# Optimization experiments

Hardware: AMD Instinct MI355X
Metric: run time of the kernel (lower is better)

## Reference

```python
import jax, jax.numpy as jnp
import numpy as np

B, F_IN, T_IN = 256, 3, 800
C, K, H, N_OUT = 128, 15, 150, 10

def hard_sigmoid(x):
    # Keras-style hard sigmoid used by LSTMHardSigmoid: clamp(0.2*x + 0.5, 0, 1)
    return jnp.clip(0.2 * x + 0.5, 0.0, 1.0)

def setup_inputs() -> dict:
    key = jax.random.key(0)
    ks = jax.random.split(key, 16)
    mk = lambda k, s, sc=0.05: (jax.random.normal(k, s, dtype=jnp.float32) * sc)
    return {
        "x": jax.random.normal(ks[0], (B, F_IN, T_IN), dtype=jnp.float32),
        "conv_w": mk(ks[1], (C, F_IN, K), 0.1),
        "conv_b": jnp.zeros((C,), jnp.float32),
        # PyTorch LSTM layout: [4H, in] with gate order i,f,g,o
        "w_ih_f": mk(ks[2], (4 * H, C)),
        "w_hh_f": mk(ks[3], (4 * H, H)),
        "b_ih_f": mk(ks[4], (4 * H,)),
        "b_hh_f": mk(ks[5], (4 * H,)),
        "w_ih_b": mk(ks[6], (4 * H, C)),
        "w_hh_b": mk(ks[7], (4 * H, H)),
        "b_ih_b": mk(ks[8], (4 * H,)),
        "b_hh_b": mk(ks[9], (4 * H,)),
        "lin1_w": mk(ks[10], (50, 2 * H)),
        "lin1_b": jnp.zeros((50,), jnp.float32),
        "lin2_w": mk(ks[11], (N_OUT, 50)),
        "lin2_b": jnp.zeros((N_OUT,), jnp.float32),
    }

def _lstm_dir(xseq, w_ih, w_hh, b_ih, b_hh, reverse):
    # xseq: [B, T, C] -> pre-activations [B, T, 4H]
    pre = jnp.einsum('btc,gc->btg', xseq, w_ih) + b_ih + b_hh
    pre_t = jnp.swapaxes(pre, 0, 1)  # [T, B, 4H]
    h0 = jnp.zeros((xseq.shape[0], H), pre.dtype)
    c0 = jnp.zeros((xseq.shape[0], H), pre.dtype)
    def step(carry, gt):
        h, c = carry
        g = gt + h @ w_hh.T
        i, f, gg, o = jnp.split(g, 4, axis=-1)
        c = hard_sigmoid(f) * c + hard_sigmoid(i) * jnp.tanh(gg)
        h = hard_sigmoid(o) * jnp.tanh(c)
        return (h, c), h
    _, hs = jax.lax.scan(step, (h0, c0), pre_t, reverse=reverse)
    return jnp.swapaxes(hs, 0, 1)  # [B, T, H]

def reference(x, conv_w, conv_b, w_ih_f, w_hh_f, b_ih_f, b_hh_f,
              w_ih_b, w_hh_b, b_ih_b, b_hh_b, lin1_w, lin1_b, lin2_w, lin2_b):
    # net1: Conv1d (VALID) + ReLU + (Dropout: identity at eval) + MaxPool1d(2)
    y = jax.lax.conv_general_dilated(
        x, conv_w, window_strides=(1,), padding='VALID',
        dimension_numbers=('NCH', 'OIH', 'NCH')) + conv_b[None, :, None]
    y = jax.nn.relu(y)                       # [B, 128, 786]
    L = y.shape[2] // 2
    y = y[:, :, :2 * L].reshape(y.shape[0], y.shape[1], L, 2).max(axis=-1)  # [B,128,393]
    xseq = jnp.transpose(y, (0, 2, 1))       # [B, 393, 128]
    # net2: bidirectional LSTM with hard-sigmoid gates
    h_fwd = _lstm_dir(xseq, w_ih_f, w_hh_f, b_ih_f, b_hh_f, reverse=False)
    h_bwd = _lstm_dir(xseq, w_ih_b, w_hh_b, b_ih_b, b_hh_b, reverse=True)
    bi = jnp.concatenate([h_fwd, h_bwd], axis=-1)  # [B, T, 300]
    # global max-pool over time (F.max_pool1d with kernel = full length)
    pooled = bi.max(axis=1)                  # [B, 300]
    # net3: Linear + ReLU + (Dropout identity) + Linear + Softmax(dim=1)
    z = jax.nn.relu(pooled @ lin1_w.T + lin1_b)
    logits = z @ lin2_w.T + lin2_b
    return jax.nn.softmax(logits, axis=1)
```

## Files before the change

kernel.cpp:

```cpp
#include <hip/hip_runtime.h>
#include <cstdio>

#define BATCH 256
#define TSEQ  393
#define CH    128
#define FIN   3
#define TIN   800
#define KK    15
#define HID   150
#define NPAD  640
#define KPAD  160
#define NB    16
#define HALF_A 197
#define HALF_B 196
#define SLOTSTRIDE (16*10240)

typedef _Float16 half_t;
typedef __attribute__((ext_vector_type(8))) _Float16 h8v;
typedef __attribute__((ext_vector_type(4))) _Float16 h4v;
typedef __attribute__((ext_vector_type(4))) float f4v;

__device__ inline float hsig(float x){ return fminf(fmaxf(fmaf(0.2f, x, 0.5f), 0.f), 1.f); }
__device__ inline float tanh_(float x){
  float e = __expf(2.f*x);
  return fmaf(-2.f, __builtin_amdgcn_rcpf(e + 1.f), 1.f);
}

#define DPPF(v, ctrl) __int_as_float(__builtin_amdgcn_mov_dpp(__float_as_int(v), ctrl, 0xF, 0xF, true))
#define XPOSE_PAIR(va, vb, om, CTRL) { float t_ = om ? va : vb; t_ = DPPF(t_, CTRL); va = om ? t_ : va; vb = om ? vb : t_; }

__global__ void prep_wih(const float* __restrict__ wf, const float* __restrict__ wb,
                         half_t* __restrict__ out){
  int i = blockIdx.x*256 + threadIdx.x;
  if (i >= 2*NPAD*CH) return;
  int c = i & 127; int n = (i >> 7) % NPAD; int d = i / (NPAD*CH);
  const float* src = d ? wb : wf;
  float v = 0.f;
  if (n < 600){ int j = n >> 2, g = n & 3; v = src[(g*HID + j)*CH + c]; }
  out[i] = (half_t)v;
}
__global__ void prep_whh(const float* __restrict__ wf, const float* __restrict__ wb,
                         half_t* __restrict__ out){
  int i = blockIdx.x*256 + threadIdx.x;
  if (i >= 2*NPAD*KPAD) return;
  int kc = i % KPAD; int n = (i / KPAD) % NPAD; int d = i / (NPAD*KPAD);
  const float* src = d ? wb : wf;
  float v = 0.f;
  if (n < 600 && kc < HID){ int j = n >> 2, g = n & 3; v = src[(g*HID + j)*HID + kc]; }
  out[i] = (half_t)v;
}
__global__ void prep_bsum(const float* __restrict__ bihf, const float* __restrict__ bhhf,
                          const float* __restrict__ bihb, const float* __restrict__ bhhb,
                          float* __restrict__ out){
  int i = blockIdx.x*256 + threadIdx.x;
  if (i >= 2*NPAD) return;
  int n = i % NPAD; int d = i / NPAD;
  float v = 0.f;
  if (n < 600){ int j = n >> 2, g = n & 3; int r = g*HID + j;
    v = d ? (bihb[r] + bhhb[r]) : (bihf[r] + bhhf[r]); }
  out[i] = v;
}

#define CTT 32
__global__ __launch_bounds__(256) void conv_pool(const float* __restrict__ x,
                                                 const float* __restrict__ w,
                                                 const float* __restrict__ bias,
                                                 half_t* __restrict__ xseq){
  __shared__ float wl[CH*FIN*KK];
  __shared__ float xl[FIN][2*CTT + 14];
  int tid = threadIdx.x;
  int b = blockIdx.x, t0 = blockIdx.y*CTT;
  for (int i = tid; i < CH*FIN*KK; i += 256) wl[i] = w[i];
  int p0 = 2*t0;
  for (int i = tid; i < FIN*(2*CTT+14); i += 256){
    int f = i/(2*CTT+14), q = i%(2*CTT+14);
    int p = p0 + q;
    xl[f][q] = (p < TIN) ? x[((size_t)b*FIN + f)*TIN + p] : 0.f;
  }
  __syncthreads();
  int c = tid & 127, th = tid >> 7;
  float a0[16], a1[16];
  #pragma unroll
  for (int i=0;i<16;++i){ a0[i]=0.f; a1[i]=0.f; }
  #pragma unroll
  for (int f=0; f<FIN; ++f){
    float xv[46];
    #pragma unroll
    for (int q=0;q<46;++q) xv[q] = xl[f][th*32 + q];
    #pragma unroll
    for (int k=0;k<KK;++k){
      float ws = wl[c*FIN*KK + f*KK + k];
      #pragma unroll
      for (int i=0;i<16;++i){
        a0[i] = fmaf(xv[2*i+k],   ws, a0[i]);
        a1[i] = fmaf(xv[2*i+k+1], ws, a1[i]);
      }
    }
  }
  float bc = bias[c];
  #pragma unroll
  for (int i=0;i<16;++i){
    int t = t0 + th*16 + i;
    if (t < TSEQ){
      float v = fmaxf(fmaxf(a0[i], a1[i]) + bc, 0.f);
      xseq[((size_t)b*TSEQ + t)*CH + c] = (half_t)v;
    }
  }
}

__global__ __launch_bounds__(512) void proj(const half_t* __restrict__ xseq,
                                            const half_t* __restrict__ wih,
                                            const float* __restrict__ bsum,
                                            half_t* __restrict__ pre,
                                            int off){
  int bt4 = blockIdx.x;
  int s   = blockIdx.y;
  int d   = blockIdx.z;
  int sg  = s + off;
  int t   = d ? (TSEQ-1 - sg) : sg;
  int tid = threadIdx.x, wv = tid >> 6, ln = tid & 63;
  int m = ln & 15, kg = ln >> 4;

  h8v bfr[5][4]; float bs[5];
  #pragma unroll
  for (int i = 0; i < 5; ++i){
    int n = (wv*5 + i)*16 + m;
    #pragma unroll
    for (int ks = 0; ks < 4; ++ks)
      bfr[i][ks] = *(const h8v*)(wih + ((size_t)d*NPAD + n)*CH + ks*32 + kg*8);
    bs[i] = bsum[d*NPAD + n];
  }
  #pragma unroll
  for (int ms = 0; ms < 4; ++ms){
    int b = bt4*64 + ms*16 + m;
    h8v ax[4];
    #pragma unroll
    for (int ks = 0; ks < 4; ++ks)
      ax[ks] = *(const h8v*)(xseq + ((size_t)b*TSEQ + t)*CH + ks*32 + kg*8);
    #pragma unroll
    for (int i = 0; i < 5; ++i){
      f4v acc = {bs[i], bs[i], bs[i], bs[i]};
      #pragma unroll
      for (int ks = 0; ks < 4; ++ks)
        acc = __builtin_amdgcn_mfma_f32_16x16x32_f16(ax[ks], bfr[i][ks], acc, 0, 0, 0);
      int n = (wv*5 + i)*16 + m;
      h4v hv = {(half_t)acc[0], (half_t)acc[1], (half_t)acc[2], (half_t)acc[3]};
      *(h4v*)(pre + (((size_t)d*HALF_A + s)*16 + (bt4*4 + ms))*10240 + n*16 + kg*4) = hv;
    }
  }
}

#define PIN4(R0,R1,R2,R3, V) asm volatile( \
  "v_accvgpr_write_b32 " R0 ", %0\n\t" \
  "v_accvgpr_write_b32 " R1 ", %1\n\t" \
  "v_accvgpr_write_b32 " R2 ", %2\n\t" \
  "v_accvgpr_write_b32 " R3 ", %3" \
  :: "v"(V[0]), "v"(V[1]), "v"(V[2]), "v"(V[3]) : R0, R1, R2, R3)

#define LP(I,KS, R0,R1,R2,R3) { \
  h8v w_ = *(const h8v*)(whh + ((size_t)d*NPAD + ((wv*5+(I))*16+m))*KPAD + (KS)*32 + kg*8); \
  f4v wf_; __builtin_memcpy(&wf_, &w_, 16); \
  PIN4(R0,R1,R2,R3, wf_); }

#define MF0(ACC, AH, AR) asm volatile("v_mfma_f32_16x16x32_f16 %0, %1, " AR ", 0"  : "=v"(ACC) : "v"(AH))
#define MF(ACC, AH, AR)  asm volatile("v_mfma_f32_16x16x32_f16 %0, %1, " AR ", %0" : "+v"(ACC) : "v"(AH))

#define ACLOBS "a0","a1","a2","a3","a4","a5","a6","a7","a8","a9",\
"a10","a11","a12","a13","a14","a15","a16","a17","a18","a19",\
"a20","a21","a22","a23","a24","a25","a26","a27","a28","a29",\
"a30","a31","a32","a33","a34","a35","a36","a37","a38","a39",\
"a40","a41","a42","a43","a44","a45","a46","a47","a48","a49",\
"a50","a51","a52","a53","a54","a55","a56","a57","a58","a59",\
"a60","a61","a62","a63","a64","a65","a66","a67","a68","a69",\
"a70","a71","a72","a73","a74","a75","a76","a77","a78","a79",\
"a80","a81","a82","a83","a84","a85","a86","a87","a88","a89",\
"a90","a91","a92","a93","a94","a95","a96","a97","a98","a99"

__global__ __launch_bounds__(512, 2) void recur(const half_t* __restrict__ pre,
                                                const half_t* __restrict__ whh,
                                                float* __restrict__ pooled,
                                                float* __restrict__ stateC,
                                                half_t* __restrict__ stateH,
                                                int first, int last, int nsteps){
  __shared__ __align__(16) half_t hbuf[2*NB*168];

  int tid = threadIdx.x, wv = tid >> 6, ln = tid & 63;
  int m = ln & 15, kg = ln >> 4;
  int bt = blockIdx.x, d = blockIdx.y;
  int b0 = bt*NB;
  int blk = d*16 + bt;
  bool o1 = (ln & 1), o2 = (ln & 2);

  LP(0,0,"a0","a1","a2","a3")    LP(0,1,"a4","a5","a6","a7")    LP(0,2,"a8","a9","a10","a11")
  LP(0,3,"a12","a13","a14","a15") LP(0,4,"a16","a17","a18","a19")
  LP(1,0,"a20","a21","a22","a23") LP(1,1,"a24","a25","a26","a27") LP(1,2,"a28","a29","a30","a31")
  LP(1,3,"a32","a33","a34","a35") LP(1,4,"a36","a37","a38","a39")
  LP(2,0,"a40","a41","a42","a43") LP(2,1,"a44","a45","a46","a47") LP(2,2,"a48","a49","a50","a51")
  LP(2,3,"a52","a53","a54","a55") LP(2,4,"a56","a57","a58","a59")
  LP(3,0,"a60","a61","a62","a63") LP(3,1,"a64","a65","a66","a67") LP(3,2,"a68","a69","a70","a71")
  LP(3,3,"a72","a73","a74","a75") LP(3,4,"a76","a77","a78","a79")
  LP(4,0,"a80","a81","a82","a83") LP(4,1,"a84","a85","a86","a87") LP(4,2,"a88","a89","a90","a91")
  LP(4,3,"a92","a93","a94","a95") LP(4,4,"a96","a97","a98","a99")

  int jc[5], bc_;
  bc_ = kg*4 + (m&3);
  #pragma unroll
  for (int T = 0; T < 5; ++T) jc[T] = 20*wv + 4*T + (m>>2);

  float c_reg[5], hm_reg[5];
  if (first){
    for (int i = tid; i < NB*168; i += 512) hbuf[i] = (half_t)0.f;
    for (int i = tid; i < NB*168; i += 512) hbuf[NB*168 + i] = (half_t)0.f;
    #pragma unroll
    for (int T = 0; T < 5; ++T){ c_reg[T] = 0.f; hm_reg[T] = -1e30f; }
  } else {
    for (int i = tid; i < NB*168; i += 512) hbuf[i] = stateH[(size_t)blk*NB*168 + i];
    for (int i = tid; i < NB*168; i += 512) hbuf[NB*168 + i] = (half_t)0.f;
    const float* sc = stateC + ((size_t)blk*512 + tid)*10;
    #pragma unroll
    for (int T = 0; T < 5; ++T){ c_reg[T] = sc[T]; hm_reg[T] = sc[5+T]; }
  }
  __syncthreads();

  const half_t* pb = pre + ((size_t)d*HALF_A*16 + bt)*10240;
  int pofl = wv*1280 + m*16 + kg*4;

  h4v curp[5], nA[5];
  #pragma unroll
  for (int T = 0; T < 5; ++T) curp[T] = *(const h4v*)(pb + pofl + T*256);
  {
    const half_t* p1 = pb + (size_t)(nsteps > 1 ? 1 : 0)*SLOTSTRIDE;
    #pragma unroll
    for (int T = 0; T < 5; ++T) nA[T] = *(const h4v*)(p1 + pofl + T*256);
  }

  int p = 0;
  #pragma unroll 1
  for (int s = 0; s < nsteps; ++s){
    int s2 = (s+2 < nsteps) ? s+2 : nsteps-1;
    const half_t* p2 = pb + (size_t)s2*SLOTSTRIDE;
    h4v nB[5];
    #pragma unroll
    for (int T = 0; T < 5; ++T) nB[T] = *(const h4v*)(p2 + pofl + T*256);

    const half_t* hrd = hbuf + p*NB*168 + m*168;
    h8v ah0 = *(const h8v*)(hrd + 0*32 + kg*8);
    h8v ah1 = *(const h8v*)(hrd + 1*32 + kg*8);
    h8v ah2 = *(const h8v*)(hrd + 2*32 + kg*8);
    h8v ah3 = *(const h8v*)(hrd + 3*32 + kg*8);
    h8v ah4 = *(const h8v*)(hrd + 4*32 + kg*8);

    f4v acc0, acc1, acc2, acc3, acc4;
    MF0(acc0, ah0, "a[0:3]");   MF0(acc1, ah0, "a[20:23]"); MF0(acc2, ah0, "a[40:43]");
    MF0(acc3, ah0, "a[60:63]"); MF0(acc4, ah0, "a[80:83]");
    MF (acc0, ah1, "a[4:7]");   MF (acc1, ah1, "a[24:27]"); MF (acc2, ah1, "a[44:47]");
    MF (acc3, ah1, "a[64:67]"); MF (acc4, ah1, "a[84:87]");
    MF (acc0, ah2, "a[8:11]");  MF (acc1, ah2, "a[28:31]"); MF (acc2, ah2, "a[48:51]");
    MF (acc3, ah2, "a[68:71]"); MF (acc4, ah2, "a[88:91]");
    MF (acc0, ah3, "a[12:15]"); MF (acc1, ah3, "a[32:35]"); MF (acc2, ah3, "a[52:55]");
    MF (acc3, ah3, "a[72:75]"); MF (acc4, ah3, "a[92:95]");
    MF (acc0, ah4, "a[16:19]"); MF (acc1, ah4, "a[36:39]"); MF (acc2, ah4, "a[56:59]");
    MF (acc3, ah4, "a[76:79]"); MF (acc4, ah4, "a[96:99]");
    asm volatile("s_nop 7\n\ts_nop 7"
                 : "+v"(acc0), "+v"(acc1), "+v"(acc2), "+v"(acc3), "+v"(acc4));

    f4v acc[5] = {acc0, acc1, acc2, acc3, acc4};
    half_t* hwr = hbuf + (p^1)*NB*168 + bc_*168;
    #pragma unroll
    for (int T = 0; T < 5; ++T){
      float v0 = acc[T][0] + (float)curp[T][0];
      float v1 = acc[T][1] + (float)curp[T][1];
      float v2 = acc[T][2] + (float)curp[T][2];
      float v3 = acc[T][3] + (float)curp[T][3];
      XPOSE_PAIR(v0, v1, o1, 0xB1);
      XPOSE_PAIR(v2, v3, o1, 0xB1);
      XPOSE_PAIR(v0, v2, o2, 0x4E);
      XPOSE_PAIR(v1, v3, o2, 0x4E);
      float cn = hsig(v1)*c_reg[T] + hsig(v0)*tanh_(v2);
      float hn = hsig(v3)*tanh_(cn);
      c_reg[T] = cn;
      hm_reg[T] = fmaxf(hm_reg[T], hn);
      hwr[jc[T]] = (half_t)hn;
    }

    #pragma unroll
    for (int T = 0; T < 5; ++T) curp[T] = nA[T];
    #pragma unroll
    for (int T = 0; T < 5; ++T) nA[T] = nB[T];

    asm volatile("s_waitcnt lgkmcnt(0)" ::: "memory", ACLOBS);
    __builtin_amdgcn_s_barrier();
    __builtin_amdgcn_sched_barrier(0);
    p ^= 1;
  }

  if (!last){
    for (int i = tid; i < NB*168; i += 512) stateH[(size_t)blk*NB*168 + i] = hbuf[p*NB*168 + i];
    float* sc = stateC + ((size_t)blk*512 + tid)*10;
    #pragma unroll
    for (int T = 0; T < 5; ++T){ sc[T] = c_reg[T]; sc[5+T] = hm_reg[T]; }
  } else {
    #pragma unroll
    for (int T = 0; T < 5; ++T){
      if (jc[T] < HID) pooled[(size_t)(b0 + bc_)*300 + d*HID + jc[T]] = hm_reg[T];
    }
  }
}

__global__ __launch_bounds__(256) void fc(const float* __restrict__ pooled,
                                          const float* __restrict__ w1, const float* __restrict__ b1,
                                          const float* __restrict__ w2, const float* __restrict__ b2,
                                          float* __restrict__ out){
  __shared__ float prow[300];
  __shared__ float ps[64][5];
  __shared__ float z[52];
  __shared__ float lg[12];
  int b = blockIdx.x, tid = threadIdx.x;
  for (int i = tid; i < 300; i += 256) prow[i] = pooled[(size_t)b*300 + i];
  __syncthreads();
  int j = tid & 63, seg = tid >> 6;
  float a = 0.f;
  if (j < 50){
    const float* wr = w1 + (size_t)j*300 + seg*75;
    const float* pr = prow + seg*75;
    #pragma unroll 5
    for (int k = 0; k < 75; ++k) a = fmaf(pr[k], wr[k], a);
  }
  ps[j][seg] = a;
  __syncthreads();
  if (tid < 50) z[tid] = fmaxf(ps[tid][0]+ps[tid][1]+ps[tid][2]+ps[tid][3] + b1[tid], 0.f);
  __syncthreads();
  if (tid < 10){
    float a2 = b2[tid];
    for (int k = 0; k < 50; ++k) a2 = fmaf(z[k], w2[tid*50 + k], a2);
    lg[tid] = a2;
  }
  __syncthreads();
  if (tid < 10){
    float mx = lg[0];
    #pragma unroll
    for (int k = 1; k < 10; ++k) mx = fmaxf(mx, lg[k]);
    float ssum = 0.f;
    #pragma unroll
    for (int k = 0; k < 10; ++k) ssum += __expf(lg[k] - mx);
    out[(size_t)b*10 + tid] = __expf(lg[tid] - mx) / ssum;
  }
}

extern "C" void kernel_launch(void* const* d_in, const int* in_sizes, int n_in,
                              void* d_out, int out_size, void* d_ws, size_t ws_size,
                              hipStream_t stream) {
  const float* x      = (const float*)d_in[0];
  const float* conv_w = (const float*)d_in[1];
  const float* conv_b = (const float*)d_in[2];
  const float* w_ih_f = (const float*)d_in[3];
  const float* w_hh_f = (const float*)d_in[4];
  const float* b_ih_f = (const float*)d_in[5];
  const float* b_hh_f = (const float*)d_in[6];
  const float* w_ih_b = (const float*)d_in[7];
  const float* w_hh_b = (const float*)d_in[8];
  const float* b_ih_b = (const float*)d_in[9];
  const float* b_hh_b = (const float*)d_in[10];
  const float* l1w = (const float*)d_in[11];
  const float* l1b = (const float*)d_in[12];
  const float* l2w = (const float*)d_in[13];
  const float* l2b = (const float*)d_in[14];
  float* out = (float*)d_out;

  char* ws = (char*)d_ws;
  size_t off = 0;
  auto alloc = [&](size_t bytes){ size_t o = off; off += (bytes + 255) & ~(size_t)255; return o; };
  size_t xseq_o = alloc((size_t)BATCH*TSEQ*CH*2);
  size_t pre_o  = alloc((size_t)2*HALF_A*16*10240*2);
  size_t wih_o  = alloc((size_t)2*NPAD*CH*2);
  size_t whh_o  = alloc((size_t)2*NPAD*KPAD*2);
  size_t bs_o   = alloc((size_t)2*NPAD*4);
  size_t pool_o = alloc((size_t)BATCH*300*4);
  size_t stc_o  = alloc((size_t)32*512*10*4);
  size_t sth_o  = alloc((size_t)32*NB*168*2);
  if (off > ws_size){
    fprintf(stderr, "[cnnblstm] WS TOO SMALL: need %zu have %zu\n", off, ws_size);
    return;
  }
  half_t* xseq_p = (half_t*)(ws + xseq_o);
  half_t* pre_p  = (half_t*)(ws + pre_o);
  half_t* wih_p  = (half_t*)(ws + wih_o);
  half_t* whh_p  = (half_t*)(ws + whh_o);
  float*  bs_p   = (float*)(ws + bs_o);
  float*  pool_p = (float*)(ws + pool_o);
  float*  stc_p  = (float*)(ws + stc_o);
  half_t* sth_p  = (half_t*)(ws + sth_o);

  prep_wih <<<(2*NPAD*CH + 255)/256, 256, 0, stream>>>(w_ih_f, w_ih_b, wih_p);
  prep_whh <<<(2*NPAD*KPAD + 255)/256, 256, 0, stream>>>(w_hh_f, w_hh_b, whh_p);
  prep_bsum<<<(2*NPAD + 255)/256, 256, 0, stream>>>(b_ih_f, b_hh_f, b_ih_b, b_hh_b, bs_p);
  conv_pool<<<dim3(BATCH, (TSEQ + CTT - 1)/CTT), 256, 0, stream>>>(x, conv_w, conv_b, xseq_p);

  proj <<<dim3(4, HALF_A, 2), 512, 0, stream>>>(xseq_p, wih_p, bs_p, pre_p, 0);
  recur<<<dim3(16, 2), 512, 0, stream>>>(pre_p, whh_p, pool_p, stc_p, sth_p, 1, 0, HALF_A);
  proj <<<dim3(4, HALF_B, 2), 512, 0, stream>>>(xseq_p, wih_p, bs_p, pre_p, HALF_A);
  recur<<<dim3(16, 2), 512, 0, stream>>>(pre_p, whh_p, pool_p, stc_p, sth_p, 0, 1, HALF_B);

  fc<<<BATCH, 256, 0, stream>>>(pool_p, l1w, l1b, l2w, l2b, out);
}
```

Before: 714.4 us.

## Pipeline input projection with recurrence across three phases and fuse setup kernels

Splits the 393-step sequence into three phases of 131 and ping-pongs two pre-activation buffers, so the input-projection MFMA blocks for the next phase run in the same launch as the 32 recurrence blocks of the current phase, using otherwise idle CUs. The pre-activation layout changes to a batch-major order with the MFMA operands swapped, which removes the DPP transposes in the gate math. The pre-activation is also loaded into the accumulator before the MFMA chain. The weight/bias prep kernels and conv are merged into one setup launch, and hard sigmoid uses fmed3. Costs include more workspace, interference between the co-resident projection blocks and the latency-bound recurrence, and an extra launch boundary.

After: 599.9 us. -16.0%, faster.

```diff
diff --git a/kernel.cpp b/kernel.cpp
--- a/kernel.cpp
+++ b/kernel.cpp
@@ -11,143 +11,142 @@
 #define NPAD  640
 #define KPAD  160
 #define NB    16
-#define HALF_A 197
-#define HALF_B 196
-#define SLOTSTRIDE (16*10240)
+#define PHASE 131
+#define SLOTSTRIDE (256*640)
 
 typedef _Float16 half_t;
 typedef __attribute__((ext_vector_type(8))) _Float16 h8v;
 typedef __attribute__((ext_vector_type(4))) _Float16 h4v;
 typedef __attribute__((ext_vector_type(4))) float f4v;
 
-__device__ inline float hsig(float x){ return fminf(fmaxf(fmaf(0.2f, x, 0.5f), 0.f), 1.f); }
+__device__ inline float hsig(float x){
+  return __builtin_amdgcn_fmed3f(fmaf(0.2f, x, 0.5f), 0.f, 1.f);
+}
 __device__ inline float tanh_(float x){
   float e = __expf(2.f*x);
   return fmaf(-2.f, __builtin_amdgcn_rcpf(e + 1.f), 1.f);
 }
 
-#define DPPF(v, ctrl) __int_as_float(__builtin_amdgcn_mov_dpp(__float_as_int(v), ctrl, 0xF, 0xF, true))
-#define XPOSE_PAIR(va, vb, om, CTRL) { float t_ = om ? va : vb; t_ = DPPF(t_, CTRL); va = om ? t_ : va; vb = om ? vb : t_; }
-
-__global__ void prep_wih(const float* __restrict__ wf, const float* __restrict__ wb,
-                         half_t* __restrict__ out){
-  int i = blockIdx.x*256 + threadIdx.x;
-  if (i >= 2*NPAD*CH) return;
-  int c = i & 127; int n = (i >> 7) % NPAD; int d = i / (NPAD*CH);
-  const float* src = d ? wb : wf;
-  float v = 0.f;
-  if (n < 600){ int j = n >> 2, g = n & 3; v = src[(g*HID + j)*CH + c]; }
-  out[i] = (half_t)v;
-}
-__global__ void prep_whh(const float* __restrict__ wf, const float* __restrict__ wb,
-                         half_t* __restrict__ out){
-  int i = blockIdx.x*256 + threadIdx.x;
-  if (i >= 2*NPAD*KPAD) return;
-  int kc = i % KPAD; int n = (i / KPAD) % NPAD; int d = i / (NPAD*KPAD);
-  const float* src = d ? wb : wf;
-  float v = 0.f;
-  if (n < 600 && kc < HID){ int j = n >> 2, g = n & 3; v = src[(g*HID + j)*HID + kc]; }
-  out[i] = (half_t)v;
-}
-__global__ void prep_bsum(const float* __restrict__ bihf, const float* __restrict__ bhhf,
-                          const float* __restrict__ bihb, const float* __restrict__ bhhb,
-                          float* __restrict__ out){
-  int i = blockIdx.x*256 + threadIdx.x;
-  if (i >= 2*NPAD) return;
-  int n = i % NPAD; int d = i / NPAD;
-  float v = 0.f;
-  if (n < 600){ int j = n >> 2, g = n & 3; int r = g*HID + j;
-    v = d ? (bihb[r] + bhhb[r]) : (bihf[r] + bhhf[r]); }
-  out[i] = v;
-}
-
-#define CTT 32
-__global__ __launch_bounds__(256) void conv_pool(const float* __restrict__ x,
-                                                 const float* __restrict__ w,
-                                                 const float* __restrict__ bias,
-                                                 half_t* __restrict__ xseq){
+__global__ __launch_bounds__(256) void setup(const float* __restrict__ x,
+    const float* __restrict__ conv_w, const float* __restrict__ conv_b,
+    const float* __restrict__ wihf, const float* __restrict__ whhf,
+    const float* __restrict__ bihf, const float* __restrict__ bhhf,
+    const float* __restrict__ wihb, const float* __restrict__ whhb,
+    const float* __restrict__ bihb, const float* __restrict__ bhhb,
+    half_t* __restrict__ xseq, half_t* __restrict__ wih, half_t* __restrict__ whh,
+    float* __restrict__ bsum){
   __shared__ float wl[CH*FIN*KK];
-  __shared__ float xl[FIN][2*CTT + 14];
-  int tid = threadIdx.x;
-  int b = blockIdx.x, t0 = blockIdx.y*CTT;
-  for (int i = tid; i < CH*FIN*KK; i += 256) wl[i] = w[i];
-  int p0 = 2*t0;
-  for (int i = tid; i < FIN*(2*CTT+14); i += 256){
-    int f = i/(2*CTT+14), q = i%(2*CTT+14);
-    int p = p0 + q;
-    xl[f][q] = (p < TIN) ? x[((size_t)b*FIN + f)*TIN + p] : 0.f;
-  }
-  __syncthreads();
-  int c = tid & 127, th = tid >> 7;
-  float a0[16], a1[16];
-  #pragma unroll
-  for (int i=0;i<16;++i){ a0[i]=0.f; a1[i]=0.f; }
-  #pragma unroll
-  for (int f=0; f<FIN; ++f){
-    float xv[46];
-    #pragma unroll
-    for (int q=0;q<46;++q) xv[q] = xl[f][th*32 + q];
-    #pragma unroll
-    for (int k=0;k<KK;++k){
-      float ws = wl[c*FIN*KK + f*KK + k];
+  __shared__ float xl[FIN][78];
+  int bx = blockIdx.x, tid = threadIdx.x;
+  if (bx < 3328){
+    int b = bx & 255, t0 = (bx >> 8)*32;
+    for (int i = tid; i < CH*FIN*KK; i += 256) wl[i] = conv_w[i];
+    int p0 = 2*t0;
+    for (int i = tid; i < FIN*78; i += 256){
+      int f = i/78, q = i%78; int p = p0 + q;
+      xl[f][q] = (p < TIN) ? x[((size_t)b*FIN + f)*TIN + p] : 0.f;
+    }
+    __syncthreads();
+    int c = tid & 127, th = tid >> 7;
+    float a0[16], a1[16];
+    #pragma unroll
+    for (int i=0;i<16;++i){ a0[i]=0.f; a1[i]=0.f; }
+    #pragma unroll
+    for (int f=0; f<FIN; ++f){
+      float xv[46];
       #pragma unroll
-      for (int i=0;i<16;++i){
-        a0[i] = fmaf(xv[2*i+k],   ws, a0[i]);
-        a1[i] = fmaf(xv[2*i+k+1], ws, a1[i]);
+      for (int q=0;q<46;++q) xv[q] = xl[f][th*32 + q];
+      #pragma unroll
+      for (int k=0;k<KK;++k){
+        float ws = wl[c*FIN*KK + f*KK + k];
+        #pragma unroll
+        for (int i=0;i<16;++i){
+          a0[i] = fmaf(xv[2*i+k],   ws, a0[i]);
+          a1[i] = fmaf(xv[2*i+k+1], ws, a1[i]);
+        }
       }
     }
-  }
-  float bc = bias[c];
-  #pragma unroll
-  for (int i=0;i<16;++i){
-    int t = t0 + th*16 + i;
-    if (t < TSEQ){
-      float v = fmaxf(fmaxf(a0[i], a1[i]) + bc, 0.f);
-      xseq[((size_t)b*TSEQ + t)*CH + c] = (half_t)v;
-    }
-  }
-}
-
-__global__ __launch_bounds__(512) void proj(const half_t* __restrict__ xseq,
-                                            const half_t* __restrict__ wih,
-                                            const float* __restrict__ bsum,
-                                            half_t* __restrict__ pre,
-                                            int off){
-  int bt4 = blockIdx.x;
-  int s   = blockIdx.y;
-  int d   = blockIdx.z;
-  int sg  = s + off;
-  int t   = d ? (TSEQ-1 - sg) : sg;
+    float bc = conv_b[c];
+    #pragma unroll
+    for (int i=0;i<16;++i){
+      int t = t0 + th*16 + i;
+      if (t < TSEQ){
+        float v = fmaxf(fmaxf(a0[i], a1[i]) + bc, 0.f);
+        xseq[((size_t)b*TSEQ + t)*CH + c] = (half_t)v;
+      }
+    }
+    return;
+  }
+  bx -= 3328;
+  if (bx < 640){
+    int i = bx*256 + tid;
+    int c = i & 127; int n = (i >> 7) % NPAD; int d = i / (NPAD*CH);
+    const float* src = d ? wihb : wihf;
+    float v = 0.f;
+    if (n < 600){ int j = n >> 2, g = n & 3; v = src[(g*HID + j)*CH + c]; }
+    wih[i] = (half_t)v;
+    return;
+  }
+  bx -= 640;
+  if (bx < 800){
+    int i = bx*256 + tid;
+    int kc = i % KPAD; int n = (i / KPAD) % NPAD; int d = i / (NPAD*KPAD);
+    const float* src = d ? whhb : whhf;
+    float v = 0.f;
+    if (n < 600 && kc < HID){ int j = n >> 2, g = n & 3; v = src[(g*HID + j)*HID + kc]; }
+    whh[i] = (half_t)v;
+    return;
+  }
+  { int i = (bx-800)*256 + tid;
+    if (i < 2*NPAD){
+      int n = i % NPAD; int d = i / NPAD;
+      float v = 0.f;
+      if (n < 600){ int j = n >> 2, g = n & 3; int r = g*HID + j;
+        v = d ? (bihb[r] + bhhb[r]) : (bihf[r] + bhhf[r]); }
+      bsum[i] = v;
+    }
+  }
+}
+
+__device__ __forceinline__ void proj_body(const half_t* __restrict__ xseq,
+    const half_t* __restrict__ wih, const float* __restrict__ bsum,
+    half_t* __restrict__ pre, int off, int nproj, int idx){
+  int bt4 = idx & 3; int rest = idx >> 2;
+  int s = rest % nproj; int d = rest / nproj;
+  int sg = s + off;
+  int t = d ? (TSEQ-1 - sg) : sg;
   int tid = threadIdx.x, wv = tid >> 6, ln = tid & 63;
   int m = ln & 15, kg = ln >> 4;
-
-  h8v bfr[5][4]; float bs[5];
+  half_t* pslot = pre + ((size_t)d*PHASE + s)*SLOTSTRIDE;
   #pragma unroll
   for (int i = 0; i < 5; ++i){
-    int n = (wv*5 + i)*16 + m;
+    int nt = (wv*5 + i)*16;
+    h8v bfr[4];
     #pragma unroll
     for (int ks = 0; ks < 4; ++ks)
-      bfr[i][ks] = *(const h8v*)(wih + ((size_t)d*NPAD + n)*CH + ks*32 + kg*8);
-    bs[i] = bsum[d*NPAD + n];
-  }
-  #pragma unroll
-  for (int ms = 0; ms < 4; ++ms){
-    int b = bt4*64 + ms*16 + m;
-    h8v ax[4];
-    #pragma unroll
-    for (int ks = 0; ks < 4; ++ks)
-      ax[ks] = *(const h8v*)(xseq + ((size_t)b*TSEQ + t)*CH + ks*32 + kg*8);
-    #pragma unroll
-    for (int i = 0; i < 5; ++i){
-      f4v acc = {bs[i], bs[i], bs[i], bs[i]};
+      bfr[ks] = *(const h8v*)(wih + ((size_t)d*NPAD + nt + m)*CH + ks*32 + kg*8);
+    f4v bs4 = *(const f4v*)(bsum + d*NPAD + nt + kg*4);
+    #pragma unroll
+    for (int ms = 0; ms < 4; ++ms){
+      int b = bt4*64 + ms*16 + m;
+      h8v ax[4];
       #pragma unroll
       for (int ks = 0; ks < 4; ++ks)
-        acc = __builtin_amdgcn_mfma_f32_16x16x32_f16(ax[ks], bfr[i][ks], acc, 0, 0, 0);
-      int n = (wv*5 + i)*16 + m;
+        ax[ks] = *(const h8v*)(xseq + ((size_t)b*TSEQ + t)*CH + ks*32 + kg*8);
+      f4v acc = bs4;
+      #pragma unroll
+      for (int ks = 0; ks < 4; ++ks)
+        acc = __builtin_amdgcn_mfma_f32_16x16x32_f16(bfr[ks], ax[ks], acc, 0, 0, 0);
       h4v hv = {(half_t)acc[0], (half_t)acc[1], (half_t)acc[2], (half_t)acc[3]};
-      *(h4v*)(pre + (((size_t)d*HALF_A + s)*16 + (bt4*4 + ms))*10240 + n*16 + kg*4) = hv;
-    }
-  }
+      *(h4v*)(pslot + (size_t)b*640 + nt + kg*4) = hv;
+    }
+  }
+}
+
+__global__ __launch_bounds__(512) void proj_kernel(const half_t* __restrict__ xseq,
+    const half_t* __restrict__ wih, const float* __restrict__ bsum,
+    half_t* __restrict__ pre, int off, int nproj){
+  proj_body(xseq, wih, bsum, pre, off, nproj, blockIdx.x);
 }
 
 #define PIN4(R0,R1,R2,R3, V) asm volatile( \
@@ -161,9 +160,6 @@
   h8v w_ = *(const h8v*)(whh + ((size_t)d*NPAD + ((wv*5+(I))*16+m))*KPAD + (KS)*32 + kg*8); \
   f4v wf_; __builtin_memcpy(&wf_, &w_, 16); \
   PIN4(R0,R1,R2,R3, wf_); }
-
-#define MF0(ACC, AH, AR) asm volatile("v_mfma_f32_16x16x32_f16 %0, %1, " AR ", 0"  : "=v"(ACC) : "v"(AH))
-#define MF(ACC, AH, AR)  asm volatile("v_mfma_f32_16x16x32_f16 %0, %1, " AR ", %0" : "+v"(ACC) : "v"(AH))
 
 #define ACLOBS "a0","a1","a2","a3","a4","a5","a6","a7","a8","a9",\
 "a10","a11","a12","a13","a14","a15","a16","a17","a18","a19",\
@@ -176,20 +172,26 @@
 "a80","a81","a82","a83","a84","a85","a86","a87","a88","a89",\
 "a90","a91","a92","a93","a94","a95","a96","a97","a98","a99"
 
-__global__ __launch_bounds__(512, 2) void recur(const half_t* __restrict__ pre,
-                                                const half_t* __restrict__ whh,
-                                                float* __restrict__ pooled,
-                                                float* __restrict__ stateC,
-                                                half_t* __restrict__ stateH,
-                                                int first, int last, int nsteps){
+__global__ __launch_bounds__(512, 2) void recur_fused(
+    const half_t* __restrict__ preR, const half_t* __restrict__ whh,
+    float* __restrict__ pooled, float* __restrict__ stateC, half_t* __restrict__ stateH,
+    int first, int last,
+    const half_t* __restrict__ xseq, const half_t* __restrict__ wih,
+    const float* __restrict__ bsum, half_t* __restrict__ preW,
+    int off_next, int nproj){
   __shared__ __align__(16) half_t hbuf[2*NB*168];
+
+  if (blockIdx.x >= 32){
+    if (nproj > 0) proj_body(xseq, wih, bsum, preW, off_next, nproj, blockIdx.x - 32);
+    return;
+  }
 
   int tid = threadIdx.x, wv = tid >> 6, ln = tid & 63;
   int m = ln & 15, kg = ln >> 4;
-  int bt = blockIdx.x, d = blockIdx.y;
+  int bl = m;
+  int bt = blockIdx.x & 15, d = blockIdx.x >> 4;
   int b0 = bt*NB;
   int blk = d*16 + bt;
-  bool o1 = (ln & 1), o2 = (ln & 2);
 
   LP(0,0,"a0","a1","a2","a3")    LP(0,1,"a4","a5","a6","a7")    LP(0,2,"a8","a9","a10","a11")
   LP(0,3,"a12","a13","a14","a15") LP(0,4,"a16","a17","a18","a19")
@@ -202,15 +204,11 @@
   LP(4,0,"a80","a81","a82","a83") LP(4,1,"a84","a85","a86","a87") LP(4,2,"a88","a89","a90","a91")
   LP(4,3,"a92","a93","a94","a95") LP(4,4,"a96","a97","a98","a99")
 
-  int jc[5], bc_;
-  bc_ = kg*4 + (m&3);
-  #pragma unroll
-  for (int T = 0; T < 5; ++T) jc[T] = 20*wv + 4*T + (m>>2);
+  int jb = wv*20 + kg;
 
   float c_reg[5], hm_reg[5];
   if (first){
-    for (int i = tid; i < NB*168; i += 512) hbuf[i] = (half_t)0.f;
-    for (int i = tid; i < NB*168; i += 512) hbuf[NB*168 + i] = (half_t)0.f;
+    for (int i = tid; i < 2*NB*168; i += 512) hbuf[i] = (half_t)0.f;
     #pragma unroll
     for (int T = 0; T < 5; ++T){ c_reg[T] = 0.f; hm_reg[T] = -1e30f; }
   } else {
@@ -222,66 +220,81 @@
   }
   __syncthreads();
 
-  const half_t* pb = pre + ((size_t)d*HALF_A*16 + bt)*10240;
-  int pofl = wv*1280 + m*16 + kg*4;
+  const half_t* pb = preR + (size_t)d*PHASE*SLOTSTRIDE + (size_t)b0*640;
+  int pofl = bl*640 + wv*80 + kg*4;
 
   h4v curp[5], nA[5];
   #pragma unroll
-  for (int T = 0; T < 5; ++T) curp[T] = *(const h4v*)(pb + pofl + T*256);
+  for (int T = 0; T < 5; ++T) curp[T] = *(const h4v*)(pb + pofl + T*16);
   {
-    const half_t* p1 = pb + (size_t)(nsteps > 1 ? 1 : 0)*SLOTSTRIDE;
-    #pragma unroll
-    for (int T = 0; T < 5; ++T) nA[T] = *(const h4v*)(p1 + pofl + T*256);
+    const half_t* p1 = pb + (size_t)SLOTSTRIDE;
+    #pragma unroll
+    for (int T = 0; T < 5; ++T) nA[T] = *(const h4v*)(p1 + pofl + T*16);
   }
 
   int p = 0;
   #pragma unroll 1
-  for (int s = 0; s < nsteps; ++s){
-    int s2 = (s+2 < nsteps) ? s+2 : nsteps-1;
+  for (int s = 0; s < PHASE; ++s){
+    int s2 = (s+2 < PHASE) ? s+2 : PHASE-1;
     const half_t* p2 = pb + (size_t)s2*SLOTSTRIDE;
     h4v nB[5];
     #pragma unroll
-    for (int T = 0; T < 5; ++T) nB[T] = *(const h4v*)(p2 + pofl + T*256);
-
-    const half_t* hrd = hbuf + p*NB*168 + m*168;
+    for (int T = 0; T < 5; ++T) nB[T] = *(const h4v*)(p2 + pofl + T*16);
+
+    const half_t* hrd = hbuf + p*NB*168 + bl*168;
     h8v ah0 = *(const h8v*)(hrd + 0*32 + kg*8);
     h8v ah1 = *(const h8v*)(hrd + 1*32 + kg*8);
     h8v ah2 = *(const h8v*)(hrd + 2*32 + kg*8);
     h8v ah3 = *(const h8v*)(hrd + 3*32 + kg*8);
     h8v ah4 = *(const h8v*)(hrd + 4*32 + kg*8);
 
-    f4v acc0, acc1, acc2, acc3, acc4;
-    MF0(acc0, ah0, "a[0:3]");   MF0(acc1, ah0, "a[20:23]"); MF0(acc2, ah0, "a[40:43]");
-    MF0(acc3, ah0, "a[60:63]"); MF0(acc4, ah0, "a[80:83]");
-    MF (acc0, ah1, "a[4:7]");   MF (acc1, ah1, "a[24:27]"); MF (acc2, ah1, "a[44:47]");
-    MF (acc3, ah1, "a[64:67]"); MF (acc4, ah1, "a[84:87]");
-    MF (acc0, ah2, "a[8:11]");  MF (acc1, ah2, "a[28:31]"); MF (acc2, ah2, "a[48:51]");
-    MF (acc3, ah2, "a[68:71]"); MF (acc4, ah2, "a[88:91]");
-    MF (acc0, ah3, "a[12:15]"); MF (acc1, ah3, "a[32:35]"); MF (acc2, ah3, "a[52:55]");
-    MF (acc3, ah3, "a[72:75]"); MF (acc4, ah3, "a[92:95]");
-    MF (acc0, ah4, "a[16:19]"); MF (acc1, ah4, "a[36:39]"); MF (acc2, ah4, "a[56:59]");
-    MF (acc3, ah4, "a[76:79]"); MF (acc4, ah4, "a[96:99]");
-    asm volatile("s_nop 7\n\ts_nop 7"
-                 : "+v"(acc0), "+v"(acc1), "+v"(acc2), "+v"(acc3), "+v"(acc4));
-
-    f4v acc[5] = {acc0, acc1, acc2, acc3, acc4};
-    half_t* hwr = hbuf + (p^1)*NB*168 + bc_*168;
-    #pragma unroll
-    for (int T = 0; T < 5; ++T){
-      float v0 = acc[T][0] + (float)curp[T][0];
-      float v1 = acc[T][1] + (float)curp[T][1];
-      float v2 = acc[T][2] + (float)curp[T][2];
-      float v3 = acc[T][3] + (float)curp[T][3];
-      XPOSE_PAIR(v0, v1, o1, 0xB1);
-      XPOSE_PAIR(v2, v3, o1, 0xB1);
-      XPOSE_PAIR(v0, v2, o2, 0x4E);
-      XPOSE_PAIR(v1, v3, o2, 0x4E);
-      float cn = hsig(v1)*c_reg[T] + hsig(v0)*tanh_(v2);
-      float hn = hsig(v3)*tanh_(cn);
-      c_reg[T] = cn;
-      hm_reg[T] = fmaxf(hm_reg[T], hn);
-      hwr[jc[T]] = (half_t)hn;
-    }
+    f4v acc0 = {(float)curp[0][0], (float)curp[0][1], (float)curp[0][2], (float)curp[0][3]};
+    f4v acc1 = {(float)curp[1][0], (float)curp[1][1], (float)curp[1][2], (float)curp[1][3]};
+    f4v acc2 = {(float)curp[2][0], (float)curp[2][1], (float)curp[2][2], (float)curp[2][3]};
+    f4v acc3 = {(float)curp[3][0], (float)curp[3][1], (float)curp[3][2], (float)curp[3][3]};
+    f4v acc4 = {(float)curp[4][0], (float)curp[4][1], (float)curp[4][2], (float)curp[4][3]};
+
+    asm volatile(
+      "s_nop 1\n\t"
+      "v_mfma_f32_16x16x32_f16 %0, a[0:3], %5, %0\n\t"
+      "v_mfma_f32_16x16x32_f16 %1, a[20:23], %5, %1\n\t"
+      "v_mfma_f32_16x16x32_f16 %2, a[40:43], %5, %2\n\t"
+      "v_mfma_f32_16x16x32_f16 %3, a[60:63], %5, %3\n\t"
+      "v_mfma_f32_16x16x32_f16 %4, a[80:83], %5, %4\n\t"
+      "v_mfma_f32_16x16x32_f16 %0, a[4:7], %6, %0\n\t"
+      "v_mfma_f32_16x16x32_f16 %1, a[24:27], %6, %1\n\t"
+      "v_mfma_f32_16x16x32_f16 %2, a[44:47], %6, %2\n\t"
+      "v_mfma_f32_16x16x32_f16 %3, a[64:67], %6, %3\n\t"
+      "v_mfma_f32_16x16x32_f16 %4, a[84:87], %6, %4\n\t"
+      "v_mfma_f32_16x16x32_f16 %0, a[8:11], %7, %0\n\t"
+      "v_mfma_f32_16x16x32_f16 %1, a[28:31], %7, %1\n\t"
+      "v_mfma_f32_16x16x32_f16 %2, a[48:51], %7, %2\n\t"
+      "v_mfma_f32_16x16x32_f16 %3, a[68:71], %7, %3\n\t"
+      "v_mfma_f32_16x16x32_f16 %4, a[88:91], %7, %4\n\t"
+      "v_mfma_f32_16x16x32_f16 %0, a[12:15], %8, %0\n\t"
+      "v_mfma_f32_16x16x32_f16 %1, a[32:35], %8, %1\n\t"
+      "v_mfma_f32_16x16x32_f16 %2, a[52:55], %8, %2\n\t"
+      "v_mfma_f32_16x16x32_f16 %3, a[72:75], %8, %3\n\t"
+      "v_mfma_f32_16x16x32_f16 %4, a[92:95], %8, %4\n\t"
+      "v_mfma_f32_16x16x32_f16 %0, a[16:19], %9, %0\n\t"
+      "v_mfma_f32_16x16x32_f16 %1, a[36:39], %9, %1\n\t"
+      "v_mfma_f32_16x16x32_f16 %2, a[56:59], %9, %2\n\t"
+      "v_mfma_f32_16x16x32_f16 %3, a[76:79], %9, %3\n\t"
+      "v_mfma_f32_16x16x32_f16 %4, a[96:99], %9, %4\n\t"
+      "s_nop 7\n\t"
+      "s_nop 7"
+      : "+v"(acc0), "+v"(acc1), "+v"(acc2), "+v"(acc3), "+v"(acc4)
+      : "v"(ah0), "v"(ah1), "v"(ah2), "v"(ah3), "v"(ah4));
+    __builtin_amdgcn_sched_barrier(0);
+
+    half_t* hwr = hbuf + (p^1)*NB*168 + bl*168 + jb;
+    #define GATE(A, T) { \
+      float cn = hsig(A[1])*c_reg[T] + hsig(A[0])*tanh_(A[2]); \
+      float hn = hsig(A[3])*tanh_(cn); \
+      c_reg[T] = cn; hm_reg[T] = fmaxf(hm_reg[T], hn); \
+      hwr[(T)*4] = (half_t)hn; }
+    GATE(acc0, 0) GATE(acc1, 1) GATE(acc2, 2) GATE(acc3, 3) GATE(acc4, 4)
+    #undef GATE
 
     #pragma unroll
     for (int T = 0; T < 5; ++T) curp[T] = nA[T];
@@ -302,7 +315,8 @@
   } else {
     #pragma unroll
     for (int T = 0; T < 5; ++T){
-      if (jc[T] < HID) pooled[(size_t)(b0 + bc_)*300 + d*HID + jc[T]] = hm_reg[T];
+      int j = jb + T*4;
+      if (j < HID) pooled[(size_t)(b0 + bl)*300 + d*HID + j] = hm_reg[T];
     }
   }
 }
@@ -371,7 +385,8 @@
   size_t off = 0;
   auto alloc = [&](size_t bytes){ size_t o = off; off += (bytes + 255) & ~(size_t)255; return o; };
   size_t xseq_o = alloc((size_t)BATCH*TSEQ*CH*2);
-  size_t pre_o  = alloc((size_t)2*HALF_A*16*10240*2);
+  size_t preA_o = alloc((size_t)2*PHASE*SLOTSTRIDE*2);
+  size_t preB_o = alloc((size_t)2*PHASE*SLOTSTRIDE*2);
   size_t wih_o  = alloc((size_t)2*NPAD*CH*2);
   size_t whh_o  = alloc((size_t)2*NPAD*KPAD*2);
   size_t bs_o   = alloc((size_t)2*NPAD*4);
@@ -383,7 +398,8 @@
     return;
   }
   half_t* xseq_p = (half_t*)(ws + xseq_o);
-  half_t* pre_p  = (half_t*)(ws + pre_o);
+  half_t* preA_p = (half_t*)(ws + preA_o);
+  half_t* preB_p = (half_t*)(ws + preB_o);
   half_t* wih_p  = (half_t*)(ws + wih_o);
   half_t* whh_p  = (half_t*)(ws + whh_o);
   float*  bs_p   = (float*)(ws + bs_o);
@@ -391,15 +407,18 @@
   float*  stc_p  = (float*)(ws + stc_o);
   half_t* sth_p  = (half_t*)(ws + sth_o);
 
-  prep_wih <<<(2*NPAD*CH + 255)/256, 256, 0, stream>>>(w_ih_f, w_ih_b, wih_p);
-  prep_whh <<<(2*NPAD*KPAD + 255)/256, 256, 0, stream>>>(w_hh_f, w_hh_b, whh_p);
-  prep_bsum<<<(2*NPAD + 255)/256, 256, 0, stream>>>(b_ih_f, b_hh_f, b_ih_b, b_hh_b, bs_p);
-  conv_pool<<<dim3(BATCH, (TSEQ + CTT - 1)/CTT), 256, 0, stream>>>(x, conv_w, conv_b, xseq_p);
-
-  proj <<<dim3(4, HALF_A, 2), 512, 0, stream>>>(xseq_p, wih_p, bs_p, pre_p, 0);
-  recur<<<dim3(16, 2), 512, 0, stream>>>(pre_p, whh_p, pool_p, stc_p, sth_p, 1, 0, HALF_A);
-  proj <<<dim3(4, HALF_B, 2), 512, 0, stream>>>(xseq_p, wih_p, bs_p, pre_p, HALF_A);
-  recur<<<dim3(16, 2), 512, 0, stream>>>(pre_p, whh_p, pool_p, stc_p, sth_p, 0, 1, HALF_B);
+  int projBlocks = 4*PHASE*2;
+
+  setup<<<3328 + 640 + 800 + 5, 256, 0, stream>>>(x, conv_w, conv_b,
+      w_ih_f, w_hh_f, b_ih_f, b_hh_f, w_ih_b, w_hh_b, b_ih_b, b_hh_b,
+      xseq_p, wih_p, whh_p, bs_p);
+  proj_kernel<<<projBlocks, 512, 0, stream>>>(xseq_p, wih_p, bs_p, preA_p, 0, PHASE);
+  recur_fused<<<32 + projBlocks, 512, 0, stream>>>(preA_p, whh_p, pool_p, stc_p, sth_p,
+      1, 0, xseq_p, wih_p, bs_p, preB_p, PHASE, PHASE);
+  recur_fused<<<32 + projBlocks, 512, 0, stream>>>(preB_p, whh_p, pool_p, stc_p, sth_p,
+      0, 0, xseq_p, wih_p, bs_p, preA_p, 2*PHASE, PHASE);
+  recur_fused<<<32, 512, 0, stream>>>(preA_p, whh_p, pool_p, stc_p, sth_p,
+      0, 1, xseq_p, wih_p, bs_p, preB_p, 0, 0);
 
   fc<<<BATCH, 256, 0, stream>>>(pool_p, l1w, l1b, l2w, l2b, out);
 }
```
